# Performance work log

Hardware: AMD Instinct MI355X
Metric: run time of the kernel (lower is better)

The kernel has to match this reference:

```python
import jax, jax.numpy as jnp
import numpy as np

B, T, D = 64, 512, 256
UNITS, MEM = 512, 64


def _glorot(key, shape):
    fan_in, fan_out = shape
    lim = np.sqrt(6.0 / (fan_in + fan_out))
    return jax.random.uniform(key, shape, jnp.float32, -lim, lim)


def setup_inputs() -> dict:
    key = jax.random.key(0)
    ks = jax.random.split(key, 12)
    return {
        "x": jax.random.normal(ks[0], (B, T, D), jnp.float32),
        "Wi": _glorot(ks[1], (D, UNITS)), "Ui": _glorot(ks[2], (UNITS, UNITS)), "bi": jnp.zeros((UNITS,), jnp.float32),
        "Wf": _glorot(ks[3], (D, UNITS)), "Uf": _glorot(ks[4], (UNITS, UNITS)), "bf": jnp.ones((UNITS,), jnp.float32),
        "Wo": _glorot(ks[5], (D, UNITS)), "Uo": _glorot(ks[6], (UNITS, UNITS)), "bo": jnp.zeros((UNITS,), jnp.float32),
        "Wc": _glorot(ks[7], (D, UNITS)), "Uc": _glorot(ks[8], (UNITS, UNITS)), "bc": jnp.zeros((UNITS,), jnp.float32),
        "Wm": _glorot(ks[9], (D, UNITS)),
        "We": _glorot(ks[10], (D, MEM)), "Ue": _glorot(ks[11], (UNITS, MEM)), "be": jnp.zeros((MEM,), jnp.float32),
    }


def _clip(v):
    return jnp.clip(v, -10.0, 10.0)


def reference(x, Wi, Ui, bi, Wf, Uf, bf, Wo, Uo, bo, Wc, Uc, bc, Wm, We, Ue, be):
    def step(carry, xt):
        h, mem = carry  # h: [B,U], mem: [B,MEM,U]
        xt = _clip(xt)
        i = jax.nn.sigmoid(_clip(xt @ Wi + h @ Ui + bi))
        f = jax.nn.sigmoid(_clip(xt @ Wf + h @ Uf + bf))
        o = jax.nn.sigmoid(_clip(xt @ Wo + h @ Uo + bo))
        c_tilde = jnp.tanh(_clip(xt @ Wc + h @ Uc + bc))
        e = jax.nn.softmax(_clip(xt @ We + h @ Ue + be), axis=-1)  # [B,MEM]
        memory_attention = jnp.sum(mem * e[:, :, None], axis=1)  # [B,U]
        c = f * (memory_attention + xt @ Wm) + i * c_tilde
        h_new = o * jnp.tanh(c)
        mem_new = jnp.concatenate([c[:, None, :], mem[:, :-1, :]], axis=1)
        return (h_new, mem_new), h_new

    h0 = jnp.zeros((x.shape[0], UNITS), x.dtype)
    m0 = jnp.zeros((x.shape[0], MEM, UNITS), x.dtype)
    (_, _), hs = jax.lax.scan(step, (h0, m0), jnp.swapaxes(x, 0, 1))
    return jnp.swapaxes(hs, 0, 1)  # [B,T,U]
```

## Files before the change

kernel.cpp:

```cpp
#include <hip/hip_runtime.h>
#include <hip/hip_bf16.h>

typedef unsigned short ushortT;
typedef __attribute__((ext_vector_type(8))) short bf16x8;
typedef __attribute__((ext_vector_type(4))) float f32x4;
typedef __attribute__((ext_vector_type(4))) int i32x4;

#define B_SZ 64
#define T_SZ 512
#define D_SZ 256
#define U_SZ 512
#define M_SZ 64

__device__ __forceinline__ ushortT f2b(float f) {
    __hip_bfloat16 h = __float2bfloat16(f);
    union { __hip_bfloat16 h; ushortT u; } c; c.h = h; return c.u;
}
__device__ __forceinline__ float clip10(float v) {
    return fminf(fmaxf(v, -10.f), 10.f);
}
__device__ __forceinline__ float tanh_fast(float z) {
    float e = __expf(2.f * z);
    return 1.f - 2.f / (e + 1.f);
}
__device__ __forceinline__ float sigm_fast(float z) {
    return 1.f / (1.f + __expf(-z));
}

__global__ void prep_xb_k(const float* __restrict__ x, ushortT* __restrict__ xb) {
    const int n4 = (B_SZ * T_SZ * D_SZ) / 4;
    for (int i = blockIdx.x * blockDim.x + threadIdx.x; i < n4; i += gridDim.x * blockDim.x) {
        float4 v = ((const float4*)x)[i];
        ushort4 o;
        o.x = f2b(clip10(v.x));
        o.y = f2b(clip10(v.y));
        o.z = f2b(clip10(v.z));
        o.w = f2b(clip10(v.w));
        ((ushort4*)xb)[i] = o;
    }
}

__global__ void prep_uw_k(const float* __restrict__ Ui, const float* __restrict__ Uf,
                          const float* __restrict__ Uo, const float* __restrict__ Uc,
                          const float* __restrict__ Ue,
                          const float* __restrict__ Wi, const float* __restrict__ Wf,
                          const float* __restrict__ Wo, const float* __restrict__ Wc,
                          const float* __restrict__ We, const float* __restrict__ Wm,
                          ushortT* __restrict__ UslT, ushortT* __restrict__ WslT) {
    const int NU = 2112 * 512;
    const int NW = 2624 * 256;
    for (int i = blockIdx.x * blockDim.x + threadIdx.x; i < NU + NW; i += gridDim.x * blockDim.x) {
        if (i < NU) {
            int c = i >> 9, k = i & 511;
            float v;
            if (c < 2048) {
                int g = c >> 9, u = c & 511;
                const float* U = (g == 0) ? Ui : (g == 1) ? Uf : (g == 2) ? Uo : Uc;
                v = U[k * 512 + u];
            } else {
                v = Ue[k * 64 + (c - 2048)];
            }
            UslT[i] = f2b(v);
        } else {
            int j = i - NU;
            int c = j >> 8, k = j & 255;
            float v;
            if (c < 2048) {
                int g = c >> 9, u = c & 511;
                const float* W = (g == 0) ? Wi : (g == 1) ? Wf : (g == 2) ? Wo : Wc;
                v = W[k * 512 + u];
            } else if (c < 2112) {
                v = We[k * 64 + (c - 2048)];
            } else {
                v = Wm[k * 512 + (c - 2112)];
            }
            WslT[j] = f2b(v);
        }
    }
}

#define MEMF_PB 1096
#define MEMF_ROW 68

__global__ __launch_bounds__(256, 1) void xlstm_rec(
    const ushortT* __restrict__ xb,
    const ushortT* __restrict__ UslT,
    const ushortT* __restrict__ WslT,
    const float* __restrict__ bi_p, const float* __restrict__ bf_p,
    const float* __restrict__ bo_p, const float* __restrict__ bc_p,
    const float* __restrict__ be_p,
    unsigned* __restrict__ Hbuf32,
    unsigned* __restrict__ Hmir,
    float* __restrict__ out)
{
    const int bid = blockIdx.x, tid = threadIdx.x;
    const int grp = bid & 7, rank = bid >> 3;
    const int wave = tid >> 6, lane = tid & 63;
    const int b0 = grp << 3;
    const int u0 = rank << 4;

    __shared__ float memF[8 * MEMF_PB];
    __shared__ float g_lds[4][8][16];
    __shared__ float e_lds[8][68];
    __shared__ float w_lds[8][72];
    __shared__ float zm_lds[8][16];
    __shared__ ushortT hLb[8][520];

    for (int i = tid; i < 8 * MEMF_PB; i += 256) memF[i] = 0.f;

    int cols[2];
    float biasv[2];
#pragma unroll
    for (int nt = 0; nt < 2; ++nt) {
        int j = wave * 32 + nt * 16 + (lane & 15);
        if (j < 64) {
            int g = j >> 4, u = u0 + (j & 15);
            cols[nt] = g * 512 + u;
            biasv[nt] = (g == 0) ? bi_p[u] : (g == 1) ? bf_p[u] : (g == 2) ? bo_p[u] : bc_p[u];
        } else {
            cols[nt] = 2048 + (j - 64);
            biasv[nt] = be_p[j - 64];
        }
    }
    const int koct = (lane >> 4) * 8;
    bf16x8 B1[2][8], B2[2][16], B1m[8];
#pragma unroll
    for (int nt = 0; nt < 2; ++nt) {
        const ushortT* bw = WslT + cols[nt] * 256;
#pragma unroll
        for (int kt = 0; kt < 8; ++kt)
            B1[nt][kt] = *(const bf16x8*)(bw + kt * 32 + koct);
        const ushortT* bu = UslT + cols[nt] * 512;
#pragma unroll
        for (int kt = 0; kt < 16; ++kt)
            B2[nt][kt] = *(const bf16x8*)(bu + kt * 32 + koct);
    }
    if (wave == 1) {
        const ushortT* bm = WslT + (2112 + u0 + (lane & 15)) * 256;
#pragma unroll
        for (int kt = 0; kt < 8; ++kt)
            B1m[kt] = *(const bf16x8*)(bm + kt * 32 + koct);
    }

    const int arow = lane & 7;
    const bool is_pw = (tid >= 64 && tid < 192);
    const int pb = (tid - 64) >> 4;
    const int pu = (tid - 64) & 15;
    const int prow = 2 * wave + (lane >> 5);
    const int pcol = (lane & 31) * 16;

    __syncthreads();

    for (int t = 0; t < T_SZ; ++t) {
        const int par = t & 1, wpar = (t + 1) & 1;
        const unsigned T16 = ((unsigned)t) << 16;

        i32x4 a1f[8];
        {
            const ushortT* xrow = xb + ((b0 + arow) * T_SZ + t) * D_SZ + koct;
#pragma unroll
            for (int kt = 0; kt < 8; ++kt)
                asm volatile("global_load_dwordx4 %0, %1, off"
                             : "=v"(a1f[kt]) : "v"(xrow + kt * 32) : "memory");
        }

        const unsigned* msrc = Hmir + (par << 15) + (b0 + prow) * 512 + pcol;
        const unsigned* hsrc = Hbuf32 + (par << 15) + (b0 + prow) * 512 + pcol;
        i32x4 g0, g1, g2, g3;
        asm volatile("global_load_dwordx4 %0, %4, off sc0\n\t"
                     "global_load_dwordx4 %1, %4, off offset:16 sc0\n\t"
                     "global_load_dwordx4 %2, %4, off offset:32 sc0\n\t"
                     "global_load_dwordx4 %3, %4, off offset:48 sc0"
                     : "=v"(g0), "=v"(g1), "=v"(g2), "=v"(g3)
                     : "v"(msrc) : "memory");
        asm volatile("s_waitcnt vmcnt(4)"
                     : "+v"(a1f[0]), "+v"(a1f[1]), "+v"(a1f[2]), "+v"(a1f[3]),
                       "+v"(a1f[4]), "+v"(a1f[5]), "+v"(a1f[6]), "+v"(a1f[7])
                     :: "memory");
        __builtin_amdgcn_sched_barrier(0);

        f32x4 acc0 = {0.f, 0.f, 0.f, 0.f}, acc1 = {0.f, 0.f, 0.f, 0.f};
        f32x4 acc2 = {0.f, 0.f, 0.f, 0.f};
#pragma unroll
        for (int kt = 0; kt < 8; ++kt) {
            bf16x8 a = __builtin_bit_cast(bf16x8, a1f[kt]);
            acc0 = __builtin_amdgcn_mfma_f32_16x16x32_bf16(a, B1[0][kt], acc0, 0, 0, 0);
            acc1 = __builtin_amdgcn_mfma_f32_16x16x32_bf16(a, B1[1][kt], acc1, 0, 0, 0);
        }
        if (wave == 1) {
#pragma unroll
            for (int kt = 0; kt < 8; ++kt) {
                bf16x8 a = __builtin_bit_cast(bf16x8, a1f[kt]);
                acc2 = __builtin_amdgcn_mfma_f32_16x16x32_bf16(a, B1m[kt], acc2, 0, 0, 0);
            }
        }

        {
            while (true) {
                asm volatile("s_waitcnt vmcnt(0)"
                             : "+v"(g0), "+v"(g1), "+v"(g2), "+v"(g3) :: "memory");
                unsigned d = (((unsigned)g0[0] ^ T16) | ((unsigned)g0[1] ^ T16)) |
                             (((unsigned)g0[2] ^ T16) | ((unsigned)g0[3] ^ T16));
                d |= (((unsigned)g1[0] ^ T16) | ((unsigned)g1[1] ^ T16)) |
                     (((unsigned)g1[2] ^ T16) | ((unsigned)g1[3] ^ T16));
                d |= (((unsigned)g2[0] ^ T16) | ((unsigned)g2[1] ^ T16)) |
                     (((unsigned)g2[2] ^ T16) | ((unsigned)g2[3] ^ T16));
                d |= (((unsigned)g3[0] ^ T16) | ((unsigned)g3[1] ^ T16)) |
                     (((unsigned)g3[2] ^ T16) | ((unsigned)g3[3] ^ T16));
                if (__all((d & 0xFFFF0000u) == 0u)) break;
                asm volatile("global_load_dwordx4 %0, %4, off sc0 sc1\n\t"
                             "global_load_dwordx4 %1, %4, off offset:16 sc0 sc1\n\t"
                             "global_load_dwordx4 %2, %4, off offset:32 sc0 sc1\n\t"
                             "global_load_dwordx4 %3, %4, off offset:48 sc0 sc1"
                             : "=v"(g0), "=v"(g1), "=v"(g2), "=v"(g3)
                             : "v"(hsrc) : "memory");
            }
        }
        __builtin_amdgcn_sched_barrier(0);

        {
            unsigned p0 = ((unsigned)g0[0] & 0xFFFFu) | ((unsigned)g0[1] << 16);
            unsigned p1 = ((unsigned)g0[2] & 0xFFFFu) | ((unsigned)g0[3] << 16);
            unsigned p2 = ((unsigned)g1[0] & 0xFFFFu) | ((unsigned)g1[1] << 16);
            unsigned p3 = ((unsigned)g1[2] & 0xFFFFu) | ((unsigned)g1[3] << 16);
            unsigned p4 = ((unsigned)g2[0] & 0xFFFFu) | ((unsigned)g2[1] << 16);
            unsigned p5 = ((unsigned)g2[2] & 0xFFFFu) | ((unsigned)g2[3] << 16);
            unsigned p6 = ((unsigned)g3[0] & 0xFFFFu) | ((unsigned)g3[1] << 16);
            unsigned p7 = ((unsigned)g3[2] & 0xFFFFu) | ((unsigned)g3[3] << 16);
            i32x4 P0 = {(int)p0, (int)p1, (int)p2, (int)p3};
            i32x4 P1 = {(int)p4, (int)p5, (int)p6, (int)p7};
            *(i32x4*)&hLb[prow][pcol] = P0;
            *(i32x4*)&hLb[prow][pcol + 8] = P1;
        }
        __syncthreads();

#pragma unroll
        for (int kt = 0; kt < 16; ++kt) {
            bf16x8 a = *(const bf16x8*)&hLb[arow][kt * 32 + koct];
            acc0 = __builtin_amdgcn_mfma_f32_16x16x32_bf16(a, B2[0][kt], acc0, 0, 0, 0);
            acc1 = __builtin_amdgcn_mfma_f32_16x16x32_bf16(a, B2[1][kt], acc1, 0, 0, 0);
        }

        if (lane < 32) {
#pragma unroll
            for (int nt = 0; nt < 2; ++nt) {
                int j = wave * 32 + nt * 16 + (lane & 15);
                f32x4 a = nt ? acc1 : acc0;
#pragma unroll
                for (int i = 0; i < 4; ++i) {
                    int b = ((lane >> 4) << 2) + i;
                    float z = clip10(a[i] + biasv[nt]);
                    if (j < 64) {
                        int g = j >> 4;
                        g_lds[g][b][j & 15] = (g == 3) ? tanh_fast(z) : sigm_fast(z);
                    } else {
                        e_lds[b][j - 64] = z;
                    }
                }
            }
            if (wave == 1) {
#pragma unroll
                for (int i = 0; i < 4; ++i)
                    zm_lds[((lane >> 4) << 2) + i][lane & 15] = acc2[i];
            }
        }
        __syncthreads();

        if (is_pw) {
            const int base = pu * 4;
            const int k0 = t - 1 - base;
            float wv0 = __expf(e_lds[pb][(unsigned)(k0) & 63]);
            float wv1 = __expf(e_lds[pb][(unsigned)(k0 - 1) & 63]);
            float wv2 = __expf(e_lds[pb][(unsigned)(k0 - 2) & 63]);
            float wv3 = __expf(e_lds[pb][(unsigned)(k0 - 3) & 63]);
            float ssum = (wv0 + wv1) + (wv2 + wv3);
#pragma unroll
            for (int d = 1; d < 16; d <<= 1) ssum += __shfl_xor(ssum, d);
            float4 wq = {wv0, wv1, wv2, wv3};
            *(float4*)&w_lds[pb][base] = wq;
            asm volatile("" ::: "memory");
            float attn = 0.f;
            const float4* wr = (const float4*)&w_lds[pb][0];
            const float4* mr = (const float4*)&memF[pb * MEMF_PB + pu * MEMF_ROW];
#pragma unroll
            for (int p4i = 0; p4i < 16; ++p4i) {
                float4 w4 = wr[p4i], m4 = mr[p4i];
                attn = fmaf(w4.x, m4.x, attn);
                attn = fmaf(w4.y, m4.y, attn);
                attn = fmaf(w4.z, m4.z, attn);
                attn = fmaf(w4.w, m4.w, attn);
            }
            attn /= ssum;
            float ig = g_lds[0][pb][pu];
            float fg = g_lds[1][pb][pu];
            float og = g_lds[2][pb][pu];
            float ct = g_lds[3][pb][pu];
            float c = fg * (attn + zm_lds[pb][pu]) + ig * ct;
            float h = og * tanh_fast(c);
            unsigned tagval = (((unsigned)(t + 1)) << 16) | (unsigned)f2b(h);
            const unsigned off = (unsigned)((wpar << 15) + (b0 + pb) * 512 + u0 + pu);
            asm volatile("global_store_dword %0, %1, off sc0"
                         :: "v"(Hmir + off), "v"(tagval) : "memory");
            asm volatile("global_store_dword %0, %1, off sc0 sc1"
                         :: "v"(Hbuf32 + off), "v"(tagval) : "memory");
            const float* oaddr = out + ((b0 + pb) * T_SZ + t) * U_SZ + u0 + pu;
            asm volatile("global_store_dword %0, %1, off"
                         :: "v"(oaddr), "v"(h) : "memory");
            memF[pb * MEMF_PB + pu * MEMF_ROW + (t & 63)] = c;
        }
    }
}

extern "C" void kernel_launch(void* const* d_in, const int* in_sizes, int n_in,
                              void* d_out, int out_size, void* d_ws, size_t ws_size,
                              hipStream_t stream) {
    const float* x  = (const float*)d_in[0];
    const float* Wi = (const float*)d_in[1];
    const float* Ui = (const float*)d_in[2];
    const float* bi = (const float*)d_in[3];
    const float* Wf = (const float*)d_in[4];
    const float* Uf = (const float*)d_in[5];
    const float* bf = (const float*)d_in[6];
    const float* Wo = (const float*)d_in[7];
    const float* Uo = (const float*)d_in[8];
    const float* bo = (const float*)d_in[9];
    const float* Wc = (const float*)d_in[10];
    const float* Uc = (const float*)d_in[11];
    const float* bc = (const float*)d_in[12];
    const float* Wm = (const float*)d_in[13];
    const float* We = (const float*)d_in[14];
    const float* Ue = (const float*)d_in[15];
    const float* be = (const float*)d_in[16];

    char* ws = (char*)d_ws;
    const size_t off_xb    = 0;
    const size_t off_uslt  = off_xb + (size_t)B_SZ * T_SZ * D_SZ * 2;
    const size_t off_wslt  = off_uslt + (size_t)2112 * 512 * 2;
    const size_t off_hbuf  = off_wslt + (size_t)2624 * 256 * 2;
    const size_t off_hmir  = off_hbuf + 262144;
    ushortT* xb       = (ushortT*)(ws + off_xb);
    ushortT* UslT     = (ushortT*)(ws + off_uslt);
    ushortT* WslT     = (ushortT*)(ws + off_wslt);
    unsigned* Hbuf32  = (unsigned*)(ws + off_hbuf);
    unsigned* Hmir    = (unsigned*)(ws + off_hmir);
    float* out = (float*)d_out;

    (void)hipMemsetAsync(ws + off_hbuf, 0, 524288, stream);

    prep_xb_k<<<2048, 256, 0, stream>>>(x, xb);
    prep_uw_k<<<2048, 256, 0, stream>>>(Ui, Uf, Uo, Uc, Ue, Wi, Wf, Wo, Wc, We, Wm,
                                        UslT, WslT);

    xlstm_rec<<<dim3(256), dim3(256), 0, stream>>>(
        xb, UslT, WslT, bi, bf, bo, bc, be, Hbuf32, Hmir, out);
}
```

Measured before the change: 1.938 ms.

## Repartition recurrent blocks to 4 batches by 32 units per block

Changes the work split of the persistent recurrent kernel: each block now handles 4 batch rows and 32 hidden units instead of 8 rows and 16 units. Each wave computes three 16-column MFMA tiles, with the e-logit columns folded in, and two waves compute the Wm projection. The hidden-state polling loop now alternates between the coherent buffer and the mirror. This is meant to cut the redundant softmax/e-logit MFMA work per block and the per-block h polling traffic. In exchange it leaves MFMA rows underused (only 4 of 16 rows valid), raises register pressure, and the unshown tail must match the new mapping.

New measurement: 1.959 ms. Within noise of the previous version (+1.1%).

```diff
diff --git a/kernel.cpp b/kernel.cpp
--- a/kernel.cpp
+++ b/kernel.cpp
@@ -79,8 +79,8 @@
     }
 }
 
-#define MEMF_PB 1096
 #define MEMF_ROW 68
+#define MEMF_PB (32 * 68 + 8)
 
 __global__ __launch_bounds__(256, 1) void xlstm_rec(
     const ushortT* __restrict__ xb,
@@ -94,38 +94,38 @@
     float* __restrict__ out)
 {
     const int bid = blockIdx.x, tid = threadIdx.x;
-    const int grp = bid & 7, rank = bid >> 3;
+    const int grp = bid & 15, rank = bid >> 4;
     const int wave = tid >> 6, lane = tid & 63;
-    const int b0 = grp << 3;
-    const int u0 = rank << 4;
-
-    __shared__ float memF[8 * MEMF_PB];
-    __shared__ float g_lds[4][8][16];
-    __shared__ float e_lds[8][68];
-    __shared__ float w_lds[8][72];
-    __shared__ float zm_lds[8][16];
-    __shared__ ushortT hLb[8][520];
-
-    for (int i = tid; i < 8 * MEMF_PB; i += 256) memF[i] = 0.f;
-
-    int cols[2];
-    float biasv[2];
-#pragma unroll
-    for (int nt = 0; nt < 2; ++nt) {
-        int j = wave * 32 + nt * 16 + (lane & 15);
-        if (j < 64) {
-            int g = j >> 4, u = u0 + (j & 15);
+    const int b0 = grp << 2;
+    const int u0 = rank << 5;
+
+    __shared__ float memF[4 * MEMF_PB];
+    __shared__ float g_lds[4][4][32];
+    __shared__ float e_lds[4][68];
+    __shared__ float w_lds[4][72];
+    __shared__ float zm_lds[4][32];
+    __shared__ ushortT hLb[4][520];
+
+    for (int i = tid; i < 4 * MEMF_PB; i += 256) memF[i] = 0.f;
+
+    int cols[3];
+    float biasv[3];
+#pragma unroll
+    for (int nt = 0; nt < 3; ++nt) {
+        int j = (wave * 3 + nt) * 16 + (lane & 15);
+        if (j < 128) {
+            int g = j >> 5, u = u0 + (j & 31);
             cols[nt] = g * 512 + u;
             biasv[nt] = (g == 0) ? bi_p[u] : (g == 1) ? bf_p[u] : (g == 2) ? bo_p[u] : bc_p[u];
         } else {
-            cols[nt] = 2048 + (j - 64);
-            biasv[nt] = be_p[j - 64];
+            cols[nt] = 2048 + (j - 128);
+            biasv[nt] = be_p[j - 128];
         }
     }
     const int koct = (lane >> 4) * 8;
-    bf16x8 B1[2][8], B2[2][16], B1m[8];
-#pragma unroll
-    for (int nt = 0; nt < 2; ++nt) {
+    bf16x8 B1[3][8], B2[3][16], B1m[8];
+#pragma unroll
+    for (int nt = 0; nt < 3; ++nt) {
         const ushortT* bw = WslT + cols[nt] * 256;
 #pragma unroll
         for (int kt = 0; kt < 8; ++kt)
@@ -135,19 +135,20 @@
         for (int kt = 0; kt < 16; ++kt)
             B2[nt][kt] = *(const bf16x8*)(bu + kt * 32 + koct);
     }
-    if (wave == 1) {
-        const ushortT* bm = WslT + (2112 + u0 + (lane & 15)) * 256;
+    if (wave == 1 || wave == 2) {
+        const ushortT* bm = WslT + (2112 + u0 + (wave - 1) * 16 + (lane & 15)) * 256;
 #pragma unroll
         for (int kt = 0; kt < 8; ++kt)
             B1m[kt] = *(const bf16x8*)(bm + kt * 32 + koct);
     }
 
-    const int arow = lane & 7;
+    const int arow = lane & 3;
     const bool is_pw = (tid >= 64 && tid < 192);
-    const int pb = (tid - 64) >> 4;
-    const int pu = (tid - 64) & 15;
-    const int prow = 2 * wave + (lane >> 5);
-    const int pcol = (lane & 31) * 16;
+    const int pb = (tid - 64) >> 5;
+    const int pu = (tid - 64) & 31;
+    const int prow = wave;
+    const int pcolg = lane * 8;
+    const int pcoll = lane * 8;
 
     __syncthreads();
 
@@ -164,30 +165,28 @@
                              : "=v"(a1f[kt]) : "v"(xrow + kt * 32) : "memory");
         }
 
-        const unsigned* msrc = Hmir + (par << 15) + (b0 + prow) * 512 + pcol;
-        const unsigned* hsrc = Hbuf32 + (par << 15) + (b0 + prow) * 512 + pcol;
-        i32x4 g0, g1, g2, g3;
-        asm volatile("global_load_dwordx4 %0, %4, off sc0\n\t"
-                     "global_load_dwordx4 %1, %4, off offset:16 sc0\n\t"
-                     "global_load_dwordx4 %2, %4, off offset:32 sc0\n\t"
-                     "global_load_dwordx4 %3, %4, off offset:48 sc0"
-                     : "=v"(g0), "=v"(g1), "=v"(g2), "=v"(g3)
-                     : "v"(msrc) : "memory");
-        asm volatile("s_waitcnt vmcnt(4)"
+        const unsigned* msrc = Hmir + (par << 15) + (b0 + prow) * 512 + pcolg;
+        const unsigned* hsrc = Hbuf32 + (par << 15) + (b0 + prow) * 512 + pcolg;
+        i32x4 g0, g1;
+        asm volatile("global_load_dwordx4 %0, %2, off sc0\n\t"
+                     "global_load_dwordx4 %1, %2, off offset:16 sc0"
+                     : "=v"(g0), "=v"(g1) : "v"(msrc) : "memory");
+        asm volatile("s_waitcnt vmcnt(2)"
                      : "+v"(a1f[0]), "+v"(a1f[1]), "+v"(a1f[2]), "+v"(a1f[3]),
                        "+v"(a1f[4]), "+v"(a1f[5]), "+v"(a1f[6]), "+v"(a1f[7])
                      :: "memory");
         __builtin_amdgcn_sched_barrier(0);
 
         f32x4 acc0 = {0.f, 0.f, 0.f, 0.f}, acc1 = {0.f, 0.f, 0.f, 0.f};
-        f32x4 acc2 = {0.f, 0.f, 0.f, 0.f};
+        f32x4 accE = {0.f, 0.f, 0.f, 0.f}, acc2 = {0.f, 0.f, 0.f, 0.f};
 #pragma unroll
         for (int kt = 0; kt < 8; ++kt) {
             bf16x8 a = __builtin_bit_cast(bf16x8, a1f[kt]);
             acc0 = __builtin_amdgcn_mfma_f32_16x16x32_bf16(a, B1[0][kt], acc0, 0, 0, 0);
             acc1 = __builtin_amdgcn_mfma_f32_16x16x32_bf16(a, B1[1][kt], acc1, 0, 0, 0);
-        }
-        if (wave == 1) {
+            accE = __builtin_amdgcn_mfma_f32_16x16x32_bf16(a, B1[2][kt], accE, 0, 0, 0);
+        }
+        if (wave == 1 || wave == 2) {
 #pragma unroll
             for (int kt = 0; kt < 8; ++kt) {
                 bf16x8 a = __builtin_bit_cast(bf16x8, a1f[kt]);
@@ -196,24 +195,25 @@
         }
 
         {
+            unsigned it = 0;
             while (true) {
                 asm volatile("s_waitcnt vmcnt(0)"
-                             : "+v"(g0), "+v"(g1), "+v"(g2), "+v"(g3) :: "memory");
+                             : "+v"(g0), "+v"(g1) :: "memory");
                 unsigned d = (((unsigned)g0[0] ^ T16) | ((unsigned)g0[1] ^ T16)) |
                              (((unsigned)g0[2] ^ T16) | ((unsigned)g0[3] ^ T16));
                 d |= (((unsigned)g1[0] ^ T16) | ((unsigned)g1[1] ^ T16)) |
                      (((unsigned)g1[2] ^ T16) | ((unsigned)g1[3] ^ T16));
-                d |= (((unsigned)g2[0] ^ T16) | ((unsigned)g2[1] ^ T16)) |
-                     (((unsigned)g2[2] ^ T16) | ((unsigned)g2[3] ^ T16));
-                d |= (((unsigned)g3[0] ^ T16) | ((unsigned)g3[1] ^ T16)) |
-                     (((unsigned)g3[2] ^ T16) | ((unsigned)g3[3] ^ T16));
                 if (__all((d & 0xFFFF0000u) == 0u)) break;
-                asm volatile("global_load_dwordx4 %0, %4, off sc0 sc1\n\t"
-                             "global_load_dwordx4 %1, %4, off offset:16 sc0 sc1\n\t"
-                             "global_load_dwordx4 %2, %4, off offset:32 sc0 sc1\n\t"
-                             "global_load_dwordx4 %3, %4, off offset:48 sc0 sc1"
-                             : "=v"(g0), "=v"(g1), "=v"(g2), "=v"(g3)
-                             : "v"(hsrc) : "memory");
+                if ((it & 1u) == 0u) {
+                    asm volatile("global_load_dwordx4 %0, %2, off sc0 sc1\n\t"
+                                 "global_load_dwordx4 %1, %2, off offset:16 sc0 sc1"
+                                 : "=v"(g0), "=v"(g1) : "v"(hsrc) : "memory");
+                } else {
+                    asm volatile("global_load_dwordx4 %0, %2, off sc0\n\t"
+                                 "global_load_dwordx4 %1, %2, off offset:16 sc0"
+                                 : "=v"(g0), "=v"(g1) : "v"(msrc) : "memory");
+                }
+                ++it;
             }
         }
         __builtin_amdgcn_sched_barrier(0);
@@ -223,14 +223,8 @@
             unsigned p1 = ((unsigned)g0[2] & 0xFFFFu) | ((unsigned)g0[3] << 16);
             unsigned p2 = ((unsigned)g1[0] & 0xFFFFu) | ((unsigned)g1[1] << 16);
             unsigned p3 = ((unsigned)g1[2] & 0xFFFFu) | ((unsigned)g1[3] << 16);
-            unsigned p4 = ((unsigned)g2[0] & 0xFFFFu) | ((unsigned)g2[1] << 16);
-            unsigned p5 = ((unsigned)g2[2] & 0xFFFFu) | ((unsigned)g2[3] << 16);
-            unsigned p6 = ((unsigned)g3[0] & 0xFFFFu) | ((unsigned)g3[1] << 16);
-            unsigned p7 = ((unsigned)g3[2] & 0xFFFFu) | ((unsigned)g3[3] << 16);
-            i32x4 P0 = {(int)p0, (int)p1, (int)p2, (int)p3};
-            i32x4 P1 = {(int)p4, (int)p5, (int)p6, (int)p7};
-            *(i32x4*)&hLb[prow][pcol] = P0;
-            *(i32x4*)&hLb[prow][pcol + 8] = P1;
+            i32x4 P = {(int)p0, (int)p1, (int)p2, (int)p3};
+            *(i32x4*)&hLb[prow][pcoll] = P;
         }
         __syncthreads();
 
@@ -239,45 +233,43 @@
             bf16x8 a = *(const bf16x8*)&hLb[arow][kt * 32 + koct];
             acc0 = __builtin_amdgcn_mfma_f32_16x16x32_bf16(a, B2[0][kt], acc0, 0, 0, 0);
             acc1 = __builtin_amdgcn_mfma_f32_16x16x32_bf16(a, B2[1][kt], acc1, 0, 0, 0);
-        }
-
-        if (lane < 32) {
-#pragma unroll
-            for (int nt = 0; nt < 2; ++nt) {
-                int j = wave * 32 + nt * 16 + (lane & 15);
-                f32x4 a = nt ? acc1 : acc0;
+            accE = __builtin_amdgcn_mfma_f32_16x16x32_bf16(a, B2[2][kt], accE, 0, 0, 0);
+        }
+
+        if (lane < 16) {
+#pragma unroll
+            for (int nt = 0; nt < 3; ++nt) {
+                int j = (wave * 3 + nt) * 16 + lane;
+                f32x4 a = (nt == 0) ? acc0 : (nt == 1) ? acc1 : accE;
 #pragma unroll
                 for (int i = 0; i < 4; ++i) {
-                    int b = ((lane >> 4) << 2) + i;
+                    int b = i;
                     float z = clip10(a[i] + biasv[nt]);
-                    if (j < 64) {
-                        int g = j >> 4;
-                        g_lds[g][b][j & 15] = (g == 3) ? tanh_fast(z) : sigm_fast(z);
+                    if (j < 128) {
+                        g_lds[j >> 5][b][j & 31] = ((j >> 5) == 3) ? tanh_fast(z) : sigm_fast(z);
                     } else {
-                        e_lds[b][j - 64] = z;
+                        e_lds[b][j - 128] = z;
                     }
                 }
             }
-            if (wave == 1) {
+            if (wave == 1 || wave == 2) {
 #pragma unroll
                 for (int i = 0; i < 4; ++i)
-                    zm_lds[((lane >> 4) << 2) + i][lane & 15] = acc2[i];
+                    zm_lds[i][(wave - 1) * 16 + lane] = acc2[i];
             }
         }
         __syncthreads();
 
         if (is_pw) {
-            const int base = pu * 4;
+            const int base = pu * 2;
             const int k0 = t - 1 - base;
             float wv0 = __expf(e_lds[pb][(unsigned)(k0) & 63]);
             float wv1 = __expf(e_lds[pb][(unsigned)(k0 - 1) & 63]);
-            float wv2 = __expf(e_lds[pb][(unsigned)(k0 - 2) & 63]);
-            float wv3 = __expf(e_lds[pb][(unsigned)(k0 - 3) & 63]);
-            float ssum = (wv0 + wv1) + (wv2 + wv3);
-#pragma unroll
-            for (int d = 1; d < 16; d <<= 1) ssum += __shfl_xor(ssum, d);
-            float4 wq = {wv0, wv1, wv2, wv3};
-            *(float4*)&w_lds[pb][base] = wq;
+            float ssum = wv0 + wv1;
+#pragma unroll
+            for (int d = 1; d < 32; d <<= 1) ssum += __shfl_xor(ssum, d);
+            float2 wq = {wv0, wv1};
+            *(float2*)&w_lds[pb][base] = wq;
             asm volatile("" ::: "memory");
             float attn = 0.f;
             const float4* wr = (const float4*)&w_lds[pb][0];
```
